# Performance work log

Measured on AMD Instinct MI355X. Metric: run time of the kernel, lower is better.

Reference implementation:

```python
import jax, jax.numpy as jnp
import numpy as np

B, N1, N2, D, H = 16, 1024, 1024, 1024, 16
DH = D // H  # head dim = 64
NEG = jnp.float32(-1e30)  # mask fill value (avoids -inf NaNs, bf16-safe)


def setup_inputs() -> dict:
    key = jax.random.key(0)
    ks = jax.random.split(key, 8)
    s = 0.02
    q = jax.random.normal(ks[0], (B, N1, D), dtype=jnp.float32)
    x = jax.random.normal(ks[1], (B, N2, D), dtype=jnp.float32)
    Wq = jax.random.normal(ks[2], (D, D), dtype=jnp.float32) * s
    Wk = jax.random.normal(ks[3], (D, D), dtype=jnp.float32) * s
    Wv = jax.random.normal(ks[4], (D, D), dtype=jnp.float32) * s
    Wo = jax.random.normal(ks[5], (D, D), dtype=jnp.float32) * s
    bq = jnp.zeros((D,), jnp.float32)
    bk = jnp.zeros((D,), jnp.float32)
    bv = jnp.zeros((D,), jnp.float32)
    bo = jnp.zeros((D,), jnp.float32)
    adj_mat = jax.random.randint(ks[6], (N1, N2), 0, 2).astype(jnp.bool_)
    return {"q": q, "x": x, "Wq": Wq, "bq": bq, "Wk": Wk, "bk": bk,
            "Wv": Wv, "bv": bv, "Wo": Wo, "bo": bo, "adj_mat": adj_mat}


def reference(q, x, Wq, bq, Wk, bk, Wv, bv, Wo, bo, adj_mat):
    b = q.shape[0]
    # QKV projections (torch Linear: y = x @ W.T + b), split into heads
    qh = (q @ Wq.T + bq).reshape(b, N1, H, DH).transpose(0, 2, 1, 3)  # [B,H,N1,DH]
    kh = (x @ Wk.T + bk).reshape(b, N2, H, DH).transpose(0, 2, 1, 3)  # [B,H,N2,DH]
    vh = (x @ Wv.T + bv).reshape(b, N2, H, DH).transpose(0, 2, 1, 3)  # [B,H,N2,DH]
    # masked SDPA with fixed adjacency mask (broadcast over batch & heads)
    scale = jnp.asarray(DH, qh.dtype) ** -0.5
    scores = jnp.einsum("bhqd,bhkd->bhqk", qh, kh) * scale           # [B,H,N1,N2]
    scores = jnp.where(adj_mat, scores, NEG)
    attn = jax.nn.softmax(scores, axis=-1)
    o = jnp.einsum("bhqk,bhkd->bhqd", attn, vh)                      # [B,H,N1,DH]
    o = o.transpose(0, 2, 1, 3).reshape(b, N1, D)
    return o @ Wo.T + bo
```

## Files before the change

### kernel.cpp

```cpp
#include <hip/hip_runtime.h>


typedef float f32x4 __attribute__((ext_vector_type(4)));
typedef __bf16 bf16x8 __attribute__((ext_vector_type(8)));

#define QSCALE 0.18033688f

__device__ __forceinline__ unsigned short f2bf(float f) {
    unsigned u = __builtin_bit_cast(unsigned, f);
    unsigned r = u + 0x7fffu + ((u >> 16) & 1u);
    return (unsigned short)(r >> 16);
}
__device__ __forceinline__ unsigned pk2(float a, float b) {
    return (unsigned)f2bf(a) | ((unsigned)f2bf(b) << 16);
}

__global__ __launch_bounds__(256) void cvt_bf16(const float* __restrict__ src,
                                                unsigned short* __restrict__ dst,
                                                int n8) {
    const int idx = blockIdx.x * 256 + threadIdx.x;
    if (idx >= n8) return;
    float4 a = ((const float4*)src)[idx * 2];
    float4 b = ((const float4*)src)[idx * 2 + 1];
    uint4 u;
    u.x = pk2(a.x, a.y); u.y = pk2(a.z, a.w);
    u.z = pk2(b.x, b.y); u.w = pk2(b.z, b.w);
    ((uint4*)dst)[idx] = u;
}

__global__ __launch_bounds__(256) void cvt_w4(const float* __restrict__ W0,
                                              const float* __restrict__ W1,
                                              const float* __restrict__ W2,
                                              const float* __restrict__ W3,
                                              unsigned short* __restrict__ o0,
                                              unsigned short* __restrict__ o1,
                                              unsigned short* __restrict__ o2,
                                              unsigned short* __restrict__ o3) {
    const float* s = (blockIdx.y == 0) ? W0 : (blockIdx.y == 1) ? W1
                   : (blockIdx.y == 2) ? W2 : W3;
    unsigned short* d = (blockIdx.y == 0) ? o0 : (blockIdx.y == 1) ? o1
                      : (blockIdx.y == 2) ? o2 : o3;
    const int idx = blockIdx.x * 256 + threadIdx.x;
    float4 a = ((const float4*)s)[idx * 2];
    float4 b = ((const float4*)s)[idx * 2 + 1];
    uint4 u;
    u.x = pk2(a.x, a.y); u.y = pk2(a.z, a.w);
    u.z = pk2(b.x, b.y); u.w = pk2(b.z, b.w);
    ((uint4*)d)[idx] = u;
}

template <int OUTM>
__global__ __launch_bounds__(256) void gemm_lds(const unsigned short* __restrict__ A,
                                                const unsigned short* __restrict__ W,
                                                const float* __restrict__ bias,
                                                void* __restrict__ Cp,
                                                float scale) {
    constexpr int N = 1024, K = 1024;
    __shared__ unsigned short As[128 * 64];
    __shared__ unsigned short Bs[128 * 64];

    const int t    = threadIdx.x;
    const int wave = t >> 6;
    const int lane = t & 63;
    const int n0   = blockIdx.x * 128;
    const int m0   = blockIdx.y * 128;
    const int wr   = (wave >> 1) * 64;
    const int wc   = (wave & 1) * 64;
    const int lm   = lane & 15;
    const int quad = lane >> 4;

    int aoff[4], boff[4];
#pragma unroll
    for (int i = 0; i < 4; i++) {
        const int slot = wave * 256 + i * 64 + lane;
        const int r = slot >> 3;
        const int csrc = (slot & 7) ^ (r & 7);
        aoff[i] = (m0 + r) * K + csrc * 8;
        boff[i] = (n0 + r) * K + csrc * 8;
    }

    f32x4 acc[4][4] = {};

    for (int k0 = 0; k0 < K; k0 += 64) {
#pragma unroll
        for (int i = 0; i < 4; i++) {
            __builtin_amdgcn_global_load_lds(
                (const __attribute__((address_space(1))) unsigned int*)(A + aoff[i] + k0),
                (__attribute__((address_space(3))) unsigned int*)((char*)As + wave * 4096 + i * 1024),
                16, 0, 0);
            __builtin_amdgcn_global_load_lds(
                (const __attribute__((address_space(1))) unsigned int*)(W + boff[i] + k0),
                (__attribute__((address_space(3))) unsigned int*)((char*)Bs + wave * 4096 + i * 1024),
                16, 0, 0);
        }
        __syncthreads();

        bf16x8 af[2][4], bfr[2][4];
#pragma unroll
        for (int ks = 0; ks < 2; ks++)
#pragma unroll
            for (int i = 0; i < 4; i++) {
                const int pos = ((ks * 4 + quad) ^ (lm & 7)) * 16;
                af[ks][i]  = *(const bf16x8*)((const char*)As + (wr + i * 16 + lm) * 128 + pos);
                bfr[ks][i] = *(const bf16x8*)((const char*)Bs + (wc + i * 16 + lm) * 128 + pos);
            }
#pragma unroll
        for (int ks = 0; ks < 2; ks++)
#pragma unroll
            for (int i = 0; i < 4; i++)
#pragma unroll
                for (int j = 0; j < 4; j++)
                    acc[i][j] = __builtin_amdgcn_mfma_f32_16x16x32_bf16(af[ks][i], bfr[ks][j],
                                                                        acc[i][j], 0, 0, 0);
        __syncthreads();
    }

#pragma unroll
    for (int i = 0; i < 4; i++) {
        const int row = m0 + wr + i * 16 + quad * 4;
#pragma unroll
        for (int j = 0; j < 4; j++) {
            const int col = n0 + wc + j * 16 + lm;
            const float bb = bias[col];
            if constexpr (OUTM == 2) {
                const int bi = row >> 10, n2 = row & 1023;
                const int hh = col >> 6, dh = col & 63;
                uint2 pkd;
                pkd.x = pk2((acc[i][j][0] + bb) * scale, (acc[i][j][1] + bb) * scale);
                pkd.y = pk2((acc[i][j][2] + bb) * scale, (acc[i][j][3] + bb) * scale);
                *(uint2*)&((unsigned short*)Cp)[((size_t)((bi * 16 + hh) * 64 + dh) << 10) + n2] = pkd;
            } else {
#pragma unroll
                for (int rr = 0; rr < 4; rr++) {
                    const float v = (acc[i][j][rr] + bb) * scale;
                    if constexpr (OUTM == 0)
                        ((unsigned short*)Cp)[(size_t)(row + rr) * N + col] = f2bf(v);
                    else
                        ((float*)Cp)[(size_t)(row + rr) * N + col] = v;
                }
            }
        }
    }
}

template <bool A_BF16, int OUTM>
__global__ __launch_bounds__(256) void gemm_bt(const void* __restrict__ Ap,
                                               const float* __restrict__ Wp,
                                               const float* __restrict__ bias,
                                               void* __restrict__ Cp,
                                               float scale) {
    constexpr int N = 1024, K = 1024;
    __shared__ unsigned short As[128 * 40];
    __shared__ unsigned short Bs[128 * 40];

    const int t    = threadIdx.x;
    const int n0   = blockIdx.x * 128;
    const int m0   = blockIdx.y * 128;
    const int wave = t >> 6;
    const int lane = t & 63;
    const int wr   = (wave >> 1) * 64;
    const int wc   = (wave & 1) * 64;
    const int lm   = lane & 15;
    const int quad = lane >> 4;
    const int kfr  = quad * 8;
    const int srow  = t >> 1;
    const int shalf = (t & 1) * 16;

    f32x4 acc[4][4] = {};

    for (int k0 = 0; k0 < K; k0 += 32) {
        {
            unsigned short* dst = &As[srow * 40 + shalf];
            if constexpr (A_BF16) {
                const unsigned short* pa =
                    (const unsigned short*)Ap + (size_t)(m0 + srow) * K + k0 + shalf;
                *(uint4*)dst       = *(const uint4*)pa;
                *(uint4*)(dst + 8) = *(const uint4*)(pa + 8);
            } else {
                const float* pa = (const float*)Ap + (size_t)(m0 + srow) * K + k0 + shalf;
                float4 f0 = *(const float4*)(pa + 0);
                float4 f1 = *(const float4*)(pa + 4);
                float4 f2 = *(const float4*)(pa + 8);
                float4 f3 = *(const float4*)(pa + 12);
                uint4 u0, u1;
                u0.x = pk2(f0.x, f0.y); u0.y = pk2(f0.z, f0.w);
                u0.z = pk2(f1.x, f1.y); u0.w = pk2(f1.z, f1.w);
                u1.x = pk2(f2.x, f2.y); u1.y = pk2(f2.z, f2.w);
                u1.z = pk2(f3.x, f3.y); u1.w = pk2(f3.z, f3.w);
                *(uint4*)dst       = u0;
                *(uint4*)(dst + 8) = u1;
            }
        }
        {
            const float* pb = Wp + (size_t)(n0 + srow) * K + k0 + shalf;
            float4 f0 = *(const float4*)(pb + 0);
            float4 f1 = *(const float4*)(pb + 4);
            float4 f2 = *(const float4*)(pb + 8);
            float4 f3 = *(const float4*)(pb + 12);
            uint4 u0, u1;
            u0.x = pk2(f0.x, f0.y); u0.y = pk2(f0.z, f0.w);
            u0.z = pk2(f1.x, f1.y); u0.w = pk2(f1.z, f1.w);
            u1.x = pk2(f2.x, f2.y); u1.y = pk2(f2.z, f2.w);
            u1.z = pk2(f3.x, f3.y); u1.w = pk2(f3.z, f3.w);
            unsigned short* dst = &Bs[srow * 40 + shalf];
            *(uint4*)dst       = u0;
            *(uint4*)(dst + 8) = u1;
        }
        __syncthreads();

        bf16x8 af[4], bfr[4];
#pragma unroll
        for (int i = 0; i < 4; i++)
            af[i] = *reinterpret_cast<const bf16x8*>(&As[(wr + i * 16 + lm) * 40 + kfr]);
#pragma unroll
        for (int j = 0; j < 4; j++)
            bfr[j] = *reinterpret_cast<const bf16x8*>(&Bs[(wc + j * 16 + lm) * 40 + kfr]);
#pragma unroll
        for (int i = 0; i < 4; i++)
#pragma unroll
            for (int j = 0; j < 4; j++)
                acc[i][j] = __builtin_amdgcn_mfma_f32_16x16x32_bf16(af[i], bfr[j],
                                                                    acc[i][j], 0, 0, 0);
        __syncthreads();
    }

#pragma unroll
    for (int i = 0; i < 4; i++) {
        const int row = m0 + wr + i * 16 + quad * 4;
#pragma unroll
        for (int j = 0; j < 4; j++) {
            const int col = n0 + wc + j * 16 + lm;
            const float bb = bias[col];
#pragma unroll
            for (int rr = 0; rr < 4; rr++) {
                const float v = (acc[i][j][rr] + bb) * scale;
                const int m = row + rr;
                if constexpr (OUTM == 0) {
                    ((unsigned short*)Cp)[(size_t)m * N + col] = f2bf(v);
                } else if constexpr (OUTM == 1) {
                    ((float*)Cp)[(size_t)m * N + col] = v;
                } else {
                    const int bi = m >> 10, n2 = m & 1023;
                    const int hh = col >> 6, dh = col & 63;
                    ((unsigned short*)Cp)[((size_t)((bi * 16 + hh) * 64 + dh) << 10) + n2] =
                        f2bf(v);
                }
            }
        }
    }
}

__global__ __launch_bounds__(256) void pack_adj(const int* __restrict__ adj,
                                                unsigned* __restrict__ adjm) {
    const int idx = blockIdx.x * 256 + threadIdx.x;
    const int* src = adj + (size_t)idx * 32;
    unsigned w = 0;
#pragma unroll
    for (int i = 0; i < 32; i++) w |= (src[i] != 0 ? 1u : 0u) << i;
    adjm[idx] = w;
}

__global__ __launch_bounds__(256, 3) void attn_kernel(const unsigned short* __restrict__ Q,
                                                      const unsigned short* __restrict__ K,
                                                      const unsigned short* __restrict__ Vt,
                                                      const unsigned* __restrict__ adjm,
                                                      unsigned short* __restrict__ O) {
    __shared__ unsigned short Kbuf[2][4096];
    __shared__ unsigned short Vbuf[2][4096];
    __shared__ unsigned short Ps[4][16][72];

    const int t    = threadIdx.x;
    const int wave = t >> 6;
    const int lane = t & 63;
    const int lml  = lane & 15;
    const int quad = lane >> 4;
    const int q0   = blockIdx.x * 128;
    const int h    = blockIdx.y;
    const int b    = blockIdx.z;

    int    ldofs[2];
    size_t kofs[2], vofs[2];
#pragma unroll
    for (int i = 0; i < 2; i++) {
        const int slot = i * 256 + t;
        const int r    = slot >> 3;
        const int cs   = (slot & 7) ^ (r & 7);
        ldofs[i] = slot * 16;
        kofs[i]  = (size_t)(b * 1024 + r) * 1024 + h * 64 + cs * 8;
        vofs[i]  = ((size_t)((b * 16 + h) * 64 + r) << 10) + cs * 8;
    }

    bf16x8 aq[2][2];
#pragma unroll
    for (int g = 0; g < 2; g++) {
        const unsigned short* qp =
            Q + ((size_t)(b * 1024 + q0 + wave * 32 + g * 16 + lml) * 1024 + h * 64 + quad * 8);
        aq[g][0] = __builtin_bit_cast(bf16x8, *(const uint4*)qp);
        aq[g][1] = __builtin_bit_cast(bf16x8, *(const uint4*)(qp + 32));
    }

    bf16x8 bones;
    {
        const unsigned short o1 = (lml == 0) ? (unsigned short)0x3F80 : (unsigned short)0;
        const unsigned oo = (unsigned)o1 | ((unsigned)o1 << 16);
        uint4 u; u.x = oo; u.y = oo; u.z = oo; u.w = oo;
        bones = __builtin_bit_cast(bf16x8, u);
    }

    f32x4 of[2][4] = {};
    f32x4 ol[2] = {};

    auto STAGE = [&](int bi, int c) {
        const size_t j0 = (size_t)c * 64;
#pragma unroll
        for (int i = 0; i < 2; i++) {
            __builtin_amdgcn_global_load_lds(
                (const __attribute__((address_space(1))) unsigned int*)(K + kofs[i] + j0 * 1024),
                (__attribute__((address_space(3))) unsigned int*)((char*)&Kbuf[bi][0] + ldofs[i]),
                16, 0, 0);
            __builtin_amdgcn_global_load_lds(
                (const __attribute__((address_space(1))) unsigned int*)(Vt + vofs[i] + j0),
                (__attribute__((address_space(3))) unsigned int*)((char*)&Vbuf[bi][0] + ldofs[i]),
                16, 0, 0);
        }
    };

    STAGE(0, 0);
    __syncthreads();

    int bi = 0;
    for (int c = 0; c < 16; ++c) {
        uint2 mw[2][4];
#pragma unroll
        for (int g = 0; g < 2; g++)
#pragma unroll
            for (int rr = 0; rr < 4; rr++) {
                const int row = q0 + wave * 32 + g * 16 + quad * 4 + rr;
                mw[g][rr] = *(const uint2*)&adjm[(size_t)row * 32 + c * 2];
            }

        if (c < 15) STAGE(bi ^ 1, c + 1);

        bf16x8 bk[4][2], bv[4][2];
#pragma unroll
        for (int f = 0; f < 4; f++)
#pragma unroll
            for (int ks = 0; ks < 2; ks++) {
                const int row = f * 16 + lml;
                const int pos = ((ks * 4 + quad) ^ (lml & 7)) * 16;
                bk[f][ks] = *(const bf16x8*)((const char*)&Kbuf[bi][0] + row * 128 + pos);
                bv[f][ks] = *(const bf16x8*)((const char*)&Vbuf[bi][0] + row * 128 + pos);
            }

#pragma unroll
        for (int g = 0; g < 2; g++) {
            f32x4 sf[4] = {};
#pragma unroll
            for (int f = 0; f < 4; f++)
#pragma unroll
                for (int ks = 0; ks < 2; ks++)
                    sf[f] = __builtin_amdgcn_mfma_f32_16x16x32_bf16(aq[g][ks], bk[f][ks],
                                                                    sf[f], 0, 0, 0);

#pragma unroll
            for (int rr = 0; rr < 4; rr++) {
                const unsigned w0 = mw[g][rr].x, w1 = mw[g][rr].y;
#pragma unroll
                for (int f = 0; f < 4; f++) {
                    const unsigned w = (f < 2) ? w0 : w1;
                    const unsigned bit = (w >> ((f * 16 + lml) & 31)) & 1u;
                    const float p = bit ? __builtin_amdgcn_exp2f(sf[f][rr]) : 0.0f;
                    Ps[wave][quad * 4 + rr][f * 16 + lml] =
                        (unsigned short)(__builtin_bit_cast(unsigned, p) >> 16);
                }
            }
            const bf16x8 ap0 = *reinterpret_cast<const bf16x8*>(&Ps[wave][lml][quad * 8]);
            const bf16x8 ap1 = *reinterpret_cast<const bf16x8*>(&Ps[wave][lml][32 + quad * 8]);

#pragma unroll
            for (int f = 0; f < 4; f++) {
                of[g][f] = __builtin_amdgcn_mfma_f32_16x16x32_bf16(ap0, bv[f][0], of[g][f], 0, 0, 0);
                of[g][f] = __builtin_amdgcn_mfma_f32_16x16x32_bf16(ap1, bv[f][1], of[g][f], 0, 0, 0);
            }
            ol[g] = __builtin_amdgcn_mfma_f32_16x16x32_bf16(ap0, bones, ol[g], 0, 0, 0);
            ol[g] = __builtin_amdgcn_mfma_f32_16x16x32_bf16(ap1, bones, ol[g], 0, 0, 0);
        }

        __syncthreads();
        bi ^= 1;
    }

#pragma unroll
    for (int g = 0; g < 2; g++) {
        float inv[4];
#pragma unroll
        for (int rr = 0; rr < 4; rr++)
            inv[rr] = 1.0f / __shfl(ol[g][rr], lane & 48);
#pragma unroll
        for (int f = 0; f < 4; f++)
#pragma unroll
            for (int rr = 0; rr < 4; rr++) {
                const size_t row = (size_t)(b * 1024 + q0 + wave * 32 + g * 16 + quad * 4 + rr);
                O[row * 1024 + h * 64 + f * 16 + lml] = f2bf(of[g][f][rr] * inv[rr]);
            }
    }
}

extern "C" void kernel_launch(void* const* d_in, const int* in_sizes, int n_in,
                              void* d_out, int out_size, void* d_ws, size_t ws_size,
                              hipStream_t stream) {
    const float* q  = (const float*)d_in[0];
    const float* x  = (const float*)d_in[1];
    const float* Wq = (const float*)d_in[2];
    const float* bq = (const float*)d_in[3];
    const float* Wk = (const float*)d_in[4];
    const float* bk = (const float*)d_in[5];
    const float* Wv = (const float*)d_in[6];
    const float* bv = (const float*)d_in[7];
    const float* Wo = (const float*)d_in[8];
    const float* bo = (const float*)d_in[9];
    const int* adj  = (const int*)d_in[10];
    float* out = (float*)d_out;

    const size_t MB = 1024 * 1024;
    const size_t NELEM = (size_t)16 * MB;
    char* w = (char*)d_ws;

    dim3 gg(8, 128), tb(256);
    const size_t FULL_WS = 168 * MB + 128 * 1024;

    if (ws_size >= FULL_WS) {
        unsigned short* qb  = (unsigned short*)(w);
        unsigned short* xb  = (unsigned short*)(w + 32 * MB);
        unsigned short* Wqb = (unsigned short*)(w + 64 * MB);
        unsigned short* Wkb = (unsigned short*)(w + 66 * MB);
        unsigned short* Wvb = (unsigned short*)(w + 68 * MB);
        unsigned short* Wob = (unsigned short*)(w + 70 * MB);
        unsigned short* Qb  = (unsigned short*)(w + 72 * MB);
        unsigned short* Kb  = (unsigned short*)(w + 104 * MB);
        unsigned short* Vtb = (unsigned short*)(w + 136 * MB);
        unsigned* adjm      = (unsigned*)(w + 168 * MB);
        unsigned short* Ob  = qb;

        hipLaunchKernelGGL(cvt_bf16, dim3(8192), tb, 0, stream, q, qb, (int)(NELEM / 8));
        hipLaunchKernelGGL(cvt_bf16, dim3(8192), tb, 0, stream, x, xb, (int)(NELEM / 8));
        hipLaunchKernelGGL(cvt_w4, dim3(512, 4), tb, 0, stream, Wq, Wk, Wv, Wo,
                           Wqb, Wkb, Wvb, Wob);
        hipLaunchKernelGGL(pack_adj, dim3(128), tb, 0, stream, adj, adjm);

        hipLaunchKernelGGL((gemm_lds<0>), gg, tb, 0, stream, qb, Wqb, bq, (void*)Qb, QSCALE);
        hipLaunchKernelGGL((gemm_lds<0>), gg, tb, 0, stream, xb, Wkb, bk, (void*)Kb, 1.0f);
        hipLaunchKernelGGL((gemm_lds<2>), gg, tb, 0, stream, xb, Wvb, bv, (void*)Vtb, 1.0f);
        hipLaunchKernelGGL(attn_kernel, dim3(8, 16, 16), tb, 0, stream, Qb, Kb, Vtb, adjm, Ob);
        hipLaunchKernelGGL((gemm_lds<1>), gg, tb, 0, stream, Ob, Wob, bo, (void*)out, 1.0f);
    } else {
        unsigned short* Qb  = (unsigned short*)(w);
        unsigned short* Kb  = (unsigned short*)(w + 32 * MB);
        unsigned short* Vtb = (unsigned short*)(w + 64 * MB);
        unsigned short* Ob  = (unsigned short*)(w + 96 * MB);
        unsigned* adjm      = (unsigned*)(w + 128 * MB);

        hipLaunchKernelGGL(pack_adj, dim3(128), tb, 0, stream, adj, adjm);
        hipLaunchKernelGGL((gemm_bt<false, 0>), gg, tb, 0, stream,
                           (const void*)q, Wq, bq, (void*)Qb, QSCALE);
        hipLaunchKernelGGL((gemm_bt<false, 0>), gg, tb, 0, stream,
                           (const void*)x, Wk, bk, (void*)Kb, 1.0f);
        hipLaunchKernelGGL((gemm_bt<false, 2>), gg, tb, 0, stream,
                           (const void*)x, Wv, bv, (void*)Vtb, 1.0f);
        hipLaunchKernelGGL(attn_kernel, dim3(8, 16, 16), tb, 0, stream, Qb, Kb, Vtb, adjm, Ob);
        hipLaunchKernelGGL((gemm_bt<true, 1>), gg, tb, 0, stream,
                           (const void*)Ob, Wo, bo, (void*)out, 1.0f);
    }
}
```

Measured before the change: 522.1 us.

## Swizzle block IDs per XCD and restructure attention inner loop with priorities

```diff
diff --git a/kernel.cpp b/kernel.cpp
--- a/kernel.cpp
+++ b/kernel.cpp
@@ -62,8 +62,11 @@
     const int t    = threadIdx.x;
     const int wave = t >> 6;
     const int lane = t & 63;
-    const int n0   = blockIdx.x * 128;
-    const int m0   = blockIdx.y * 128;
+    const int bid  = blockIdx.x;
+    const int xcd  = bid & 7;
+    const int jj   = bid >> 3;
+    const int n0   = (jj & 7) * 128;
+    const int m0   = (xcd * 16 + (jj >> 3)) * 128;
     const int wr   = (wave >> 1) * 64;
     const int wc   = (wave & 1) * 64;
     const int lm   = lane & 15;
@@ -267,16 +270,21 @@
                                                       unsigned short* __restrict__ O) {
     __shared__ unsigned short Kbuf[2][4096];
     __shared__ unsigned short Vbuf[2][4096];
-    __shared__ unsigned short Ps[4][16][72];
+    __shared__ unsigned short Ps[4][2][16][72];
 
     const int t    = threadIdx.x;
     const int wave = t >> 6;
     const int lane = t & 63;
     const int lml  = lane & 15;
     const int quad = lane >> 4;
-    const int q0   = blockIdx.x * 128;
-    const int h    = blockIdx.y;
-    const int b    = blockIdx.z;
+
+    const int bid   = blockIdx.x;
+    const int xcd   = bid & 7;
+    const int jj    = bid >> 3;
+    const int group = xcd * 32 + (jj >> 3);
+    const int q0    = (jj & 7) * 128;
+    const int h     = group & 15;
+    const int b     = group >> 4;
 
     int    ldofs[2];
     size_t kofs[2], vofs[2];
@@ -341,7 +349,7 @@
 
         if (c < 15) STAGE(bi ^ 1, c + 1);
 
-        bf16x8 bk[4][2], bv[4][2];
+        bf16x8 bk[4][2];
 #pragma unroll
         for (int f = 0; f < 4; f++)
 #pragma unroll
@@ -349,34 +357,51 @@
                 const int row = f * 16 + lml;
                 const int pos = ((ks * 4 + quad) ^ (lml & 7)) * 16;
                 bk[f][ks] = *(const bf16x8*)((const char*)&Kbuf[bi][0] + row * 128 + pos);
-                bv[f][ks] = *(const bf16x8*)((const char*)&Vbuf[bi][0] + row * 128 + pos);
-            }
-
-#pragma unroll
-        for (int g = 0; g < 2; g++) {
-            f32x4 sf[4] = {};
+            }
+
+        f32x4 sf[2][4] = {};
+        __builtin_amdgcn_s_setprio(1);
+#pragma unroll
+        for (int g = 0; g < 2; g++)
 #pragma unroll
             for (int f = 0; f < 4; f++)
 #pragma unroll
                 for (int ks = 0; ks < 2; ks++)
-                    sf[f] = __builtin_amdgcn_mfma_f32_16x16x32_bf16(aq[g][ks], bk[f][ks],
-                                                                    sf[f], 0, 0, 0);
-
+                    sf[g][f] = __builtin_amdgcn_mfma_f32_16x16x32_bf16(aq[g][ks], bk[f][ks],
+                                                                       sf[g][f], 0, 0, 0);
+        __builtin_amdgcn_s_setprio(0);
+
+#pragma unroll
+        for (int g = 0; g < 2; g++)
 #pragma unroll
             for (int rr = 0; rr < 4; rr++) {
-                const unsigned w0 = mw[g][rr].x, w1 = mw[g][rr].y;
+                const unsigned w0s = mw[g][rr].x >> lml;
+                const unsigned w1s = mw[g][rr].y >> lml;
 #pragma unroll
                 for (int f = 0; f < 4; f++) {
-                    const unsigned w = (f < 2) ? w0 : w1;
-                    const unsigned bit = (w >> ((f * 16 + lml) & 31)) & 1u;
-                    const float p = bit ? __builtin_amdgcn_exp2f(sf[f][rr]) : 0.0f;
-                    Ps[wave][quad * 4 + rr][f * 16 + lml] =
+                    const unsigned ws  = (f < 2) ? w0s : w1s;
+                    const unsigned bit = (f & 1) ? ((ws >> 16) & 1u) : (ws & 1u);
+                    const float p = bit ? __builtin_amdgcn_exp2f(sf[g][f][rr]) : 0.0f;
+                    Ps[wave][g][quad * 4 + rr][f * 16 + lml] =
                         (unsigned short)(__builtin_bit_cast(unsigned, p) >> 16);
                 }
             }
-            const bf16x8 ap0 = *reinterpret_cast<const bf16x8*>(&Ps[wave][lml][quad * 8]);
-            const bf16x8 ap1 = *reinterpret_cast<const bf16x8*>(&Ps[wave][lml][32 + quad * 8]);
-
+
+        bf16x8 bv[4][2];
+#pragma unroll
+        for (int f = 0; f < 4; f++)
+#pragma unroll
+            for (int ks = 0; ks < 2; ks++) {
+                const int row = f * 16 + lml;
+                const int pos = ((ks * 4 + quad) ^ (lml & 7)) * 16;
+                bv[f][ks] = *(const bf16x8*)((const char*)&Vbuf[bi][0] + row * 128 + pos);
+            }
+
+#pragma unroll
+        for (int g = 0; g < 2; g++) {
+            const bf16x8 ap0 = *reinterpret_cast<const bf16x8*>(&Ps[wave][g][lml][quad * 8]);
+            const bf16x8 ap1 = *reinterpret_cast<const bf16x8*>(&Ps[wave][g][lml][32 + quad * 8]);
+            __builtin_amdgcn_s_setprio(1);
 #pragma unroll
             for (int f = 0; f < 4; f++) {
                 of[g][f] = __builtin_amdgcn_mfma_f32_16x16x32_bf16(ap0, bv[f][0], of[g][f], 0, 0, 0);
@@ -384,6 +409,7 @@
             }
             ol[g] = __builtin_amdgcn_mfma_f32_16x16x32_bf16(ap0, bones, ol[g], 0, 0, 0);
             ol[g] = __builtin_amdgcn_mfma_f32_16x16x32_bf16(ap1, bones, ol[g], 0, 0, 0);
+            __builtin_amdgcn_s_setprio(0);
         }
 
         __syncthreads();
@@ -426,7 +452,7 @@
     const size_t NELEM = (size_t)16 * MB;
     char* w = (char*)d_ws;
 
-    dim3 gg(8, 128), tb(256);
+    dim3 gswz(1024), tb(256);
     const size_t FULL_WS = 168 * MB + 128 * 1024;
 
     if (ws_size >= FULL_WS) {
@@ -448,11 +474,11 @@
                            Wqb, Wkb, Wvb, Wob);
         hipLaunchKernelGGL(pack_adj, dim3(128), tb, 0, stream, adj, adjm);
 
-        hipLaunchKernelGGL((gemm_lds<0>), gg, tb, 0, stream, qb, Wqb, bq, (void*)Qb, QSCALE);
-        hipLaunchKernelGGL((gemm_lds<0>), gg, tb, 0, stream, xb, Wkb, bk, (void*)Kb, 1.0f);
-        hipLaunchKernelGGL((gemm_lds<2>), gg, tb, 0, stream, xb, Wvb, bv, (void*)Vtb, 1.0f);
-        hipLaunchKernelGGL(attn_kernel, dim3(8, 16, 16), tb, 0, stream, Qb, Kb, Vtb, adjm, Ob);
-        hipLaunchKernelGGL((gemm_lds<1>), gg, tb, 0, stream, Ob, Wob, bo, (void*)out, 1.0f);
+        hipLaunchKernelGGL((gemm_lds<0>), gswz, tb, 0, stream, qb, Wqb, bq, (void*)Qb, QSCALE);
+        hipLaunchKernelGGL((gemm_lds<0>), gswz, tb, 0, stream, xb, Wkb, bk, (void*)Kb, 1.0f);
+        hipLaunchKernelGGL((gemm_lds<2>), gswz, tb, 0, stream, xb, Wvb, bv, (void*)Vtb, 1.0f);
+        hipLaunchKernelGGL(attn_kernel, dim3(2048), tb, 0, stream, Qb, Kb, Vtb, adjm, Ob);
+        hipLaunchKernelGGL((gemm_lds<1>), gswz, tb, 0, stream, Ob, Wob, bo, (void*)out, 1.0f);
     } else {
         unsigned short* Qb  = (unsigned short*)(w);
         unsigned short* Kb  = (unsigned short*)(w + 32 * MB);
@@ -461,14 +487,14 @@
         unsigned* adjm      = (unsigned*)(w + 128 * MB);
 
         hipLaunchKernelGGL(pack_adj, dim3(128), tb, 0, stream, adj, adjm);
-        hipLaunchKernelGGL((gemm_bt<false, 0>), gg, tb, 0, stream,
+        hipLaunchKernelGGL((gemm_bt<false, 0>), dim3(8, 128), tb, 0, stream,
                            (const void*)q, Wq, bq, (void*)Qb, QSCALE);
-        hipLaunchKernelGGL((gemm_bt<false, 0>), gg, tb, 0, stream,
+        hipLaunchKernelGGL((gemm_bt<false, 0>), dim3(8, 128), tb, 0, stream,
                            (const void*)x, Wk, bk, (void*)Kb, 1.0f);
-        hipLaunchKernelGGL((gemm_bt<false, 2>), gg, tb, 0, stream,
+        hipLaunchKernelGGL((gemm_bt<false, 2>), dim3(8, 128), tb, 0, stream,
                            (const void*)x, Wv, bv, (void*)Vtb, 1.0f);
-        hipLaunchKernelGGL(attn_kernel, dim3(8, 16, 16), tb, 0, stream, Qb, Kb, Vtb, adjm, Ob);
-        hipLaunchKernelGGL((gemm_bt<true, 1>), gg, tb, 0, stream,
+        hipLaunchKernelGGL(attn_kernel, dim3(2048), tb, 0, stream, Qb, Kb, Vtb, adjm, Ob);
+        hipLaunchKernelGGL((gemm_bt<true, 1>), dim3(8, 128), tb, 0, stream,
                            (const void*)Ob, Wo, bo, (void*)out, 1.0f);
     }
 }
```

Result: faster. 480.9 us (-7.9%).
